# Optimization experiments

Hardware: AMD Instinct MI355X
Metric: run time of the kernel (lower is better)

The kernel has to match this reference:

```python
import jax, jax.numpy as jnp
import numpy as np

NUM_HEAD = 8
HIDDEN = 1024


def setup_inputs() -> dict:
    key = jax.random.key(0)
    ks = jax.random.split(key, 7)
    B, Q, K = 2, 256, 256
    return {
        "query": jax.random.normal(ks[0], (B, Q, HIDDEN), jnp.float32),
        "keys": jax.random.normal(ks[1], (B, K, HIDDEN), jnp.float32),
        "values": jax.random.normal(ks[2], (B, K, HIDDEN), jnp.float32),
        "mask": jax.random.randint(ks[3], (B, K), 0, 2, jnp.int32),
        "W_q": jax.random.normal(ks[4], (HIDDEN, HIDDEN), jnp.float32),
        "W_k": jax.random.normal(ks[5], (HIDDEN, HIDDEN), jnp.float32),
        "V_a": jax.random.normal(ks[6], (HIDDEN,), jnp.float32),
    }


def reference(query, keys, values, mask, W_q, W_k, V_a):
    B, Q, H = query.shape
    K = keys.shape[1]
    h_q = query @ W_q                                   # [B,Q,H]
    h_k = keys @ W_k                                    # [B,K,H]
    # additive (Bahdanau) scores, split hidden into heads and sum per head
    h = jnp.tanh(h_q[:, :, None, :] + h_k[:, None, :, :]) * V_a   # [B,Q,K,H]
    logits = h.reshape(B, Q, K, NUM_HEAD, H // NUM_HEAD).sum(-1)  # [B,Q,K,h]
    logits = jnp.transpose(logits, (0, 3, 1, 2))        # [B,h,Q,K]
    penalty = (1.0 - mask.astype(jnp.float32)) * 99.0   # [B,K]
    logits = logits - penalty[:, None, None, :]
    weights = jax.nn.softmax(logits, axis=-1)           # [B,h,Q,K]
    v = values.reshape(B, K, NUM_HEAD, H // NUM_HEAD)   # [B,K,h,d]
    ctx = jnp.einsum('bhqk,bkhd->bqhd', weights, v).reshape(B, Q, H)
    return ctx, weights
```

## Files before the change

kernel.cpp:

```cpp
#include <hip/hip_runtime.h>
#include <hip/hip_bf16.h>


#define TANH_SCALE 2.88539008177792681472f
#define LOG2E      1.44269504088896340736f

typedef __attribute__((ext_vector_type(8))) short bf16x8_t;
typedef __attribute__((ext_vector_type(4))) float f32x4_t;

__device__ inline ushort bf16_rne(float f) {
  unsigned u = __float_as_uint(f);
  u += 0x7FFFu + ((u >> 16) & 1u);
  return (ushort)(u >> 16);
}
__device__ inline float bf16_to_f(ushort h) { return __uint_as_float((unsigned)h << 16); }
__device__ inline void split1(float v, ushort& hi, ushort& lo) {
  hi = bf16_rne(v);
  lo = bf16_rne(v - bf16_to_f(hi));
}

__global__ __launch_bounds__(256) void prep(
    const float* __restrict__ query, const float* __restrict__ keys,
    const float* __restrict__ Wq, const float* __restrict__ Wk,
    ushort* __restrict__ qhi, ushort* __restrict__ qlo,
    ushort* __restrict__ khi, ushort* __restrict__ klo,
    ushort* __restrict__ wqthi, ushort* __restrict__ wqtlo,
    ushort* __restrict__ wkthi, ushort* __restrict__ wktlo)
{
  __shared__ float t[64][65];
  const int bid = blockIdx.x, tid = threadIdx.x;
  if (bid < 1024) {
    const int z = bid >> 9;
    const float* in = z ? keys : query;
    ushort* hi = z ? khi : qhi;
    ushort* lo = z ? klo : qlo;
    const size_t i = ((size_t)(bid & 511) * 256 + tid) * 4;
    float4 v = *(const float4*)(in + i);
    ushort h0, h1, h2, h3, l0, l1, l2, l3;
    split1(v.x, h0, l0); split1(v.y, h1, l1);
    split1(v.z, h2, l2); split1(v.w, h3, l3);
    *(ushort4*)(hi + i) = make_ushort4(h0, h1, h2, h3);
    *(ushort4*)(lo + i) = make_ushort4(l0, l1, l2, l3);
  } else {
    const int idx = bid - 1024;
    const int z = idx >> 8;
    const float* W = z ? Wk : Wq;
    ushort* thi = z ? wkthi : wqthi;
    ushort* tlo = z ? wktlo : wqtlo;
    const int n0 = (idx & 15) * 64, h0 = ((idx >> 4) & 15) * 64;
    const int r = tid >> 4, c = (tid & 15) * 4;
#pragma unroll
    for (int i = 0; i < 4; ++i) {
      const int rr = r + i * 16;
      float4 wv = *(const float4*)(W + (size_t)(h0 + rr) * 1024 + n0 + c);
      t[rr][c + 0] = wv.x; t[rr][c + 1] = wv.y;
      t[rr][c + 2] = wv.z; t[rr][c + 3] = wv.w;
    }
    __syncthreads();
#pragma unroll
    for (int i = 0; i < 4; ++i) {
      const int rr = r + i * 16;
      ushort h0v, h1v, h2v, h3v, l0v, l1v, l2v, l3v;
      split1(t[c + 0][rr] * TANH_SCALE, h0v, l0v);
      split1(t[c + 1][rr] * TANH_SCALE, h1v, l1v);
      split1(t[c + 2][rr] * TANH_SCALE, h2v, l2v);
      split1(t[c + 3][rr] * TANH_SCALE, h3v, l3v);
      *(ushort4*)(thi + (size_t)(n0 + rr) * 1024 + h0 + c) = make_ushort4(h0v, h1v, h2v, h3v);
      *(ushort4*)(tlo + (size_t)(n0 + rr) * 1024 + h0 + c) = make_ushort4(l0v, l1v, l2v, l3v);
    }
  }
}

__global__ __launch_bounds__(256) void gemm_mfma(
    const ushort* __restrict__ qhi, const ushort* __restrict__ qlo,
    const ushort* __restrict__ khi, const ushort* __restrict__ klo,
    const ushort* __restrict__ wqthi, const ushort* __restrict__ wqtlo,
    const ushort* __restrict__ wkthi, const ushort* __restrict__ wktlo,
    float* __restrict__ hq_f, float* __restrict__ hkT)
{
  const int z = blockIdx.y;
  const int bid = blockIdx.x;
  int m0, n0, ldc;
  const ushort *Ah_g, *Al_g, *Bh_g, *Bl_g;
  float* C;
  if (z == 0) {
    m0 = (bid >> 4) * 64; n0 = (bid & 15) * 64; ldc = 1024;
    Ah_g = qhi; Al_g = qlo; Bh_g = wqthi; Bl_g = wqtlo; C = hq_f;
  } else {
    m0 = (bid >> 3) * 64; n0 = (bid & 7) * 64; ldc = 512;
    Ah_g = wkthi; Al_g = wktlo; Bh_g = khi; Bl_g = klo; C = hkT;
  }

  __shared__ __align__(16) ushort Ah[64 * 40];
  __shared__ __align__(16) ushort Al[64 * 40];
  __shared__ __align__(16) ushort Bh[64 * 40];
  __shared__ __align__(16) ushort Bl[64 * 40];

  const int tid = threadIdx.x;
  const int srow = tid >> 2, skc = (tid & 3) * 8;
  const size_t gA = (size_t)(m0 + srow) * 1024 + skc;
  const size_t gB = (size_t)(n0 + srow) * 1024 + skc;
  const int soff = srow * 40 + skc;

  uint4 rah = *(const uint4*)(Ah_g + gA);
  uint4 ral = *(const uint4*)(Al_g + gA);
  uint4 rbh = *(const uint4*)(Bh_g + gB);
  uint4 rbl = *(const uint4*)(Bl_g + gB);

  const int w = __builtin_amdgcn_readfirstlane(tid >> 6);
  const int lane = tid & 63;
  const int wm = (w >> 1) * 32, wn = (w & 1) * 32;
  const int fr = lane & 15, kg = lane >> 4;
  const int aoff = (wm + fr) * 40 + kg * 8;
  const int boff = (wn + fr) * 40 + kg * 8;

  f32x4_t acc[2][2] = {};

  for (int kk = 0; kk < 1024; kk += 32) {
    __syncthreads();
    *(uint4*)(Ah + soff) = rah;
    *(uint4*)(Al + soff) = ral;
    *(uint4*)(Bh + soff) = rbh;
    *(uint4*)(Bl + soff) = rbl;
    __syncthreads();

    if (kk + 32 < 1024) {
      rah = *(const uint4*)(Ah_g + gA + kk + 32);
      ral = *(const uint4*)(Al_g + gA + kk + 32);
      rbh = *(const uint4*)(Bh_g + gB + kk + 32);
      rbl = *(const uint4*)(Bl_g + gB + kk + 32);
    }

    bf16x8_t ah0 = *(const bf16x8_t*)(Ah + aoff);
    bf16x8_t ah1 = *(const bf16x8_t*)(Ah + aoff + 16 * 40);
    bf16x8_t al0 = *(const bf16x8_t*)(Al + aoff);
    bf16x8_t al1 = *(const bf16x8_t*)(Al + aoff + 16 * 40);
    bf16x8_t bh0 = *(const bf16x8_t*)(Bh + boff);
    bf16x8_t bh1 = *(const bf16x8_t*)(Bh + boff + 16 * 40);
    bf16x8_t bl0 = *(const bf16x8_t*)(Bl + boff);
    bf16x8_t bl1 = *(const bf16x8_t*)(Bl + boff + 16 * 40);

    acc[0][0] = __builtin_amdgcn_mfma_f32_16x16x32_bf16(ah0, bh0, acc[0][0], 0, 0, 0);
    acc[0][1] = __builtin_amdgcn_mfma_f32_16x16x32_bf16(ah0, bh1, acc[0][1], 0, 0, 0);
    acc[1][0] = __builtin_amdgcn_mfma_f32_16x16x32_bf16(ah1, bh0, acc[1][0], 0, 0, 0);
    acc[1][1] = __builtin_amdgcn_mfma_f32_16x16x32_bf16(ah1, bh1, acc[1][1], 0, 0, 0);
    acc[0][0] = __builtin_amdgcn_mfma_f32_16x16x32_bf16(ah0, bl0, acc[0][0], 0, 0, 0);
    acc[0][1] = __builtin_amdgcn_mfma_f32_16x16x32_bf16(ah0, bl1, acc[0][1], 0, 0, 0);
    acc[1][0] = __builtin_amdgcn_mfma_f32_16x16x32_bf16(ah1, bl0, acc[1][0], 0, 0, 0);
    acc[1][1] = __builtin_amdgcn_mfma_f32_16x16x32_bf16(ah1, bl1, acc[1][1], 0, 0, 0);
    acc[0][0] = __builtin_amdgcn_mfma_f32_16x16x32_bf16(al0, bh0, acc[0][0], 0, 0, 0);
    acc[0][1] = __builtin_amdgcn_mfma_f32_16x16x32_bf16(al0, bh1, acc[0][1], 0, 0, 0);
    acc[1][0] = __builtin_amdgcn_mfma_f32_16x16x32_bf16(al1, bh0, acc[1][0], 0, 0, 0);
    acc[1][1] = __builtin_amdgcn_mfma_f32_16x16x32_bf16(al1, bh1, acc[1][1], 0, 0, 0);
  }

#pragma unroll
  for (int fm = 0; fm < 2; ++fm)
#pragma unroll
    for (int fn = 0; fn < 2; ++fn) {
      const int col = n0 + wn + fn * 16 + fr;
#pragma unroll
      for (int j = 0; j < 4; ++j) {
        const int row = m0 + wm + fm * 16 + kg * 4 + j;
        C[(size_t)row * ldc + col] = acc[fm][fn][j];
      }
    }
}

#define COMP(vk, hq0v, hq1v, vad)                                     \
  {                                                                   \
    float e0 = __builtin_amdgcn_exp2f(hq0v + vk.x);                   \
    float e1 = __builtin_amdgcn_exp2f(hq0v + vk.y);                   \
    float e2 = __builtin_amdgcn_exp2f(hq0v + vk.z);                   \
    float e3 = __builtin_amdgcn_exp2f(hq0v + vk.w);                   \
    acc00 += vad * __builtin_amdgcn_rcpf(e0 + 1.0f);                  \
    acc01 += vad * __builtin_amdgcn_rcpf(e1 + 1.0f);                  \
    acc02 += vad * __builtin_amdgcn_rcpf(e2 + 1.0f);                  \
    acc03 += vad * __builtin_amdgcn_rcpf(e3 + 1.0f);                  \
    float f0 = __builtin_amdgcn_exp2f(hq1v + vk.x);                   \
    float f1 = __builtin_amdgcn_exp2f(hq1v + vk.y);                   \
    float f2 = __builtin_amdgcn_exp2f(hq1v + vk.z);                   \
    float f3 = __builtin_amdgcn_exp2f(hq1v + vk.w);                   \
    acc10 += vad * __builtin_amdgcn_rcpf(f0 + 1.0f);                  \
    acc11 += vad * __builtin_amdgcn_rcpf(f1 + 1.0f);                  \
    acc12 += vad * __builtin_amdgcn_rcpf(f2 + 1.0f);                  \
    acc13 += vad * __builtin_amdgcn_rcpf(f3 + 1.0f);                  \
  }

__global__ __launch_bounds__(256) void attn_fused(
    const float* __restrict__ hq_f, const float* __restrict__ hkT,
    const float* __restrict__ Va, const int* __restrict__ mask,
    const float* __restrict__ values,
    float* __restrict__ weights, float* __restrict__ ctx)
{
  __shared__ __align__(16) float w_lds[8 * 256];
  const int tid = threadIdx.x;
  const int lane = tid & 63;
  const int w = __builtin_amdgcn_readfirstlane(tid >> 6);
  const int bid = blockIdx.x;
  const int hb = bid >> 5;
  const int b = hb & 1, h = hb >> 1;
  const int qt = (bid & 31) * 8;
  const int q0 = qt + w * 2;

  int4 mk = *(const int4*)(mask + b * 256 + 4 * lane);
  const float pen0 = 99.0f * (1.0f - (float)mk.x);
  const float pen1 = 99.0f * (1.0f - (float)mk.y);
  const float pen2 = 99.0f * (1.0f - (float)mk.z);
  const float pen3 = 99.0f * (1.0f - (float)mk.w);

  float ssum = Va[h * 128 + lane] + Va[h * 128 + 64 + lane];
#pragma unroll
  for (int off = 32; off; off >>= 1) ssum += __shfl_xor(ssum, off, 64);

  const float* hkbase = hkT + (size_t)(h * 128) * 512 + b * 256 + 4 * lane;
  const float* hqr0 = hq_f + (size_t)(b * 256 + q0) * 1024 + h * 128;
  const float* hqr1 = hqr0 + 1024;
  const float* vap = Va + h * 128;

  float acc00 = 0.f, acc01 = 0.f, acc02 = 0.f, acc03 = 0.f;
  float acc10 = 0.f, acc11 = 0.f, acc12 = 0.f, acc13 = 0.f;

  float4 vk0 = *(const float4*)(hkbase + 0 * 512);
  float4 vk1 = *(const float4*)(hkbase + 1 * 512);
  float4 vk2 = *(const float4*)(hkbase + 2 * 512);
  float4 vk3 = *(const float4*)(hkbase + 3 * 512);
  float4 hqA = *(const float4*)(hqr0);
  float4 hqB = *(const float4*)(hqr1);
  float4 va4 = *(const float4*)(vap);

  for (int g = 0; g < 32; ++g) {
    float4 nvk0, nvk1, nvk2, nvk3, nhqA, nhqB, nva4;
    if (g < 31) {
      const float* hb2 = hkbase + (size_t)(4 * g + 4) * 512;
      nvk0 = *(const float4*)(hb2 + 0 * 512);
      nvk1 = *(const float4*)(hb2 + 1 * 512);
      nvk2 = *(const float4*)(hb2 + 2 * 512);
      nvk3 = *(const float4*)(hb2 + 3 * 512);
      nhqA = *(const float4*)(hqr0 + 4 * g + 4);
      nhqB = *(const float4*)(hqr1 + 4 * g + 4);
      nva4 = *(const float4*)(vap + 4 * g + 4);
    }
    COMP(vk0, hqA.x, hqB.x, va4.x);
    COMP(vk1, hqA.y, hqB.y, va4.y);
    COMP(vk2, hqA.z, hqB.z, va4.z);
    COMP(vk3, hqA.w, hqB.w, va4.w);
    if (g < 31) {
      vk0 = nvk0; vk1 = nvk1; vk2 = nvk2; vk3 = nvk3;
      hqA = nhqA; hqB = nhqB; va4 = nva4;
    }
  }

  float4 L0, L1;
  L0.x = ssum - 2.0f * acc00 - pen0;
  L0.y = ssum - 2.0f * acc01 - pen1;
  L0.z = ssum - 2.0f * acc02 - pen2;
  L0.w = ssum - 2.0f * acc03 - pen3;
  L1.x = ssum - 2.0f * acc10 - pen0;
  L1.y = ssum - 2.0f * acc11 - pen1;
  L1.z = ssum - 2.0f * acc12 - pen2;
  L1.w = ssum - 2.0f * acc13 - pen3;

  float m0 = fmaxf(fmaxf(L0.x, L0.y), fmaxf(L0.z, L0.w));
  float m1 = fmaxf(fmaxf(L1.x, L1.y), fmaxf(L1.z, L1.w));
#pragma unroll
  for (int off = 32; off; off >>= 1) {
    m0 = fmaxf(m0, __shfl_xor(m0, off, 64));
    m1 = fmaxf(m1, __shfl_xor(m1, off, 64));
  }
  float4 P0, P1;
  P0.x = __builtin_amdgcn_exp2f((L0.x - m0) * LOG2E);
  P0.y = __builtin_amdgcn_exp2f((L0.y - m0) * LOG2E);
  P0.z = __builtin_amdgcn_exp2f((L0.z - m0) * LOG2E);
  P0.w = __builtin_amdgcn_exp2f((L0.w - m0) * LOG2E);
  P1.x = __builtin_amdgcn_exp2f((L1.x - m1) * LOG2E);
  P1.y = __builtin_amdgcn_exp2f((L1.y - m1) * LOG2E);
  P1.z = __builtin_amdgcn_exp2f((L1.z - m1) * LOG2E);
  P1.w = __builtin_amdgcn_exp2f((L1.w - m1) * LOG2E);
  float s0 = (P0.x + P0.y) + (P0.z + P0.w);
  float s1 = (P1.x + P1.y) + (P1.z + P1.w);
#pragma unroll
  for (int off = 32; off; off >>= 1) {
    s0 += __shfl_xor(s0, off, 64);
    s1 += __shfl_xor(s1, off, 64);
  }
  float inv0 = 1.0f / s0, inv1 = 1.0f / s1;
  P0.x *= inv0; P0.y *= inv0; P0.z *= inv0; P0.w *= inv0;
  P1.x *= inv1; P1.y *= inv1; P1.z *= inv1; P1.w *= inv1;

  float* wp = weights + ((size_t)((b * 8 + h) * 256) + q0) * 256 + 4 * lane;
  *(float4*)(wp) = P0;
  *(float4*)(wp + 256) = P1;
  *(float4*)&w_lds[(w * 2 + 0) * 256 + 4 * lane] = P0;
  *(float4*)&w_lds[(w * 2 + 1) * 256 + 4 * lane] = P1;
  __syncthreads();

  const int q = tid >> 5, dq = tid & 31;
  const float* vb = values + (size_t)(b * 256) * 1024 + h * 128 + dq * 4;
  const float* wrow = w_lds + q * 256;
  float4 accE = make_float4(0, 0, 0, 0), accO = make_float4(0, 0, 0, 0);
#pragma unroll 4
  for (int k = 0; k < 256; k += 2) {
    float4 v0 = *(const float4*)&vb[k * 1024];
    float4 v1 = *(const float4*)&vb[(k + 1) * 1024];
    float w0 = wrow[k], w1 = wrow[k + 1];
    accE.x += w0 * v0.x; accE.y += w0 * v0.y; accE.z += w0 * v0.z; accE.w += w0 * v0.w;
    accO.x += w1 * v1.x; accO.y += w1 * v1.y; accO.z += w1 * v1.z; accO.w += w1 * v1.w;
  }
  float4 o;
  o.x = accE.x + accO.x; o.y = accE.y + accO.y; o.z = accE.z + accO.z; o.w = accE.w + accO.w;
  *(float4*)&ctx[(size_t)(b * 256 + qt + q) * 1024 + h * 128 + dq * 4] = o;
}

extern "C" void kernel_launch(void* const* d_in, const int* in_sizes, int n_in,
                              void* d_out, int out_size, void* d_ws, size_t ws_size,
                              hipStream_t stream) {
  const float* query  = (const float*)d_in[0];
  const float* keys   = (const float*)d_in[1];
  const float* values = (const float*)d_in[2];
  const int*   mask   = (const int*)d_in[3];
  const float* Wq     = (const float*)d_in[4];
  const float* Wk     = (const float*)d_in[5];
  const float* Va     = (const float*)d_in[6];

  float* ctx     = (float*)d_out;
  float* weights = ctx + 524288;

  ushort* qhi   = (ushort*)d_ws;
  ushort* qlo   = qhi + 524288;
  ushort* khi   = qlo + 524288;
  ushort* klo   = khi + 524288;
  ushort* wqthi = klo + 524288;
  ushort* wqtlo = wqthi + 1048576;
  ushort* wkthi = wqtlo + 1048576;
  ushort* wktlo = wkthi + 1048576;
  float*  hq_f  = (float*)(wktlo + 1048576);
  float*  hkT   = hq_f + 524288;

  prep<<<dim3(1536), 256, 0, stream>>>(query, keys, Wq, Wk,
                                       qhi, qlo, khi, klo,
                                       wqthi, wqtlo, wkthi, wktlo);
  gemm_mfma<<<dim3(128, 2), 256, 0, stream>>>(qhi, qlo, khi, klo,
                                              wqthi, wqtlo, wkthi, wktlo, hq_f, hkT);
  attn_fused<<<dim3(512), 256, 0, stream>>>(hq_f, hkT, Va, mask, values, weights, ctx);
}
```

Measured before the change: 73.10 us.

## Split attention work across more blocks with key-halved waves and cross-wave reductions

Each block now handles 2 queries instead of 8, and the two waves per query each cover half of the keys (2 keys per lane instead of 4 keys across 2 queries). Softmax max and sum are combined across wave pairs through shared memory, and the PV product is split over key quarters with a shuffle plus LDS reduction. This raises the grid from 512 to 2048 blocks to improve occupancy and latency hiding in the tanh-heavy score loop. In exchange, the hq and hk loads are reused less, synchronisation goes up, and the weight stores are narrower.

```diff
diff --git a/kernel.cpp b/kernel.cpp
--- a/kernel.cpp
+++ b/kernel.cpp
@@ -167,149 +167,139 @@
     }
 }
 
-#define COMP(vk, hq0v, hq1v, vad)                                     \
-  {                                                                   \
-    float e0 = __builtin_amdgcn_exp2f(hq0v + vk.x);                   \
-    float e1 = __builtin_amdgcn_exp2f(hq0v + vk.y);                   \
-    float e2 = __builtin_amdgcn_exp2f(hq0v + vk.z);                   \
-    float e3 = __builtin_amdgcn_exp2f(hq0v + vk.w);                   \
-    acc00 += vad * __builtin_amdgcn_rcpf(e0 + 1.0f);                  \
-    acc01 += vad * __builtin_amdgcn_rcpf(e1 + 1.0f);                  \
-    acc02 += vad * __builtin_amdgcn_rcpf(e2 + 1.0f);                  \
-    acc03 += vad * __builtin_amdgcn_rcpf(e3 + 1.0f);                  \
-    float f0 = __builtin_amdgcn_exp2f(hq1v + vk.x);                   \
-    float f1 = __builtin_amdgcn_exp2f(hq1v + vk.y);                   \
-    float f2 = __builtin_amdgcn_exp2f(hq1v + vk.z);                   \
-    float f3 = __builtin_amdgcn_exp2f(hq1v + vk.w);                   \
-    acc10 += vad * __builtin_amdgcn_rcpf(f0 + 1.0f);                  \
-    acc11 += vad * __builtin_amdgcn_rcpf(f1 + 1.0f);                  \
-    acc12 += vad * __builtin_amdgcn_rcpf(f2 + 1.0f);                  \
-    acc13 += vad * __builtin_amdgcn_rcpf(f3 + 1.0f);                  \
-  }
-
 __global__ __launch_bounds__(256) void attn_fused(
     const float* __restrict__ hq_f, const float* __restrict__ hkT,
     const float* __restrict__ Va, const int* __restrict__ mask,
     const float* __restrict__ values,
     float* __restrict__ weights, float* __restrict__ ctx)
 {
-  __shared__ __align__(16) float w_lds[8 * 256];
+  __shared__ float red_m[4];
+  __shared__ float red_s[4];
+  __shared__ __align__(16) float w_lds[2][256];
+  __shared__ __align__(16) float pv_part[4][32][4];
+
   const int tid = threadIdx.x;
   const int lane = tid & 63;
   const int w = __builtin_amdgcn_readfirstlane(tid >> 6);
+  const int r = w >> 1, kh = w & 1;
   const int bid = blockIdx.x;
-  const int hb = bid >> 5;
-  const int b = hb & 1, h = hb >> 1;
-  const int qt = (bid & 31) * 8;
-  const int q0 = qt + w * 2;
-
-  int4 mk = *(const int4*)(mask + b * 256 + 4 * lane);
+  const int bh = bid >> 7;
+  const int b = bh & 1, h = bh >> 1;
+  const int q = (bid & 127) * 2 + r;
+  const int k0 = kh * 128 + 2 * lane;
+
+  const int2 mk = *(const int2*)(mask + b * 256 + k0);
   const float pen0 = 99.0f * (1.0f - (float)mk.x);
   const float pen1 = 99.0f * (1.0f - (float)mk.y);
-  const float pen2 = 99.0f * (1.0f - (float)mk.z);
-  const float pen3 = 99.0f * (1.0f - (float)mk.w);
 
   float ssum = Va[h * 128 + lane] + Va[h * 128 + 64 + lane];
 #pragma unroll
   for (int off = 32; off; off >>= 1) ssum += __shfl_xor(ssum, off, 64);
 
-  const float* hkbase = hkT + (size_t)(h * 128) * 512 + b * 256 + 4 * lane;
-  const float* hqr0 = hq_f + (size_t)(b * 256 + q0) * 1024 + h * 128;
-  const float* hqr1 = hqr0 + 1024;
+  const float* ekb = hkT + (size_t)(h * 128) * 512 + b * 256 + k0;
+  const float* hqp = hq_f + (size_t)(b * 256 + q) * 1024 + h * 128;
   const float* vap = Va + h * 128;
 
-  float acc00 = 0.f, acc01 = 0.f, acc02 = 0.f, acc03 = 0.f;
-  float acc10 = 0.f, acc11 = 0.f, acc12 = 0.f, acc13 = 0.f;
-
-  float4 vk0 = *(const float4*)(hkbase + 0 * 512);
-  float4 vk1 = *(const float4*)(hkbase + 1 * 512);
-  float4 vk2 = *(const float4*)(hkbase + 2 * 512);
-  float4 vk3 = *(const float4*)(hkbase + 3 * 512);
-  float4 hqA = *(const float4*)(hqr0);
-  float4 hqB = *(const float4*)(hqr1);
+  float a0e = 0.f, a0o = 0.f, a1e = 0.f, a1o = 0.f;
+
+  float2 e0 = *(const float2*)(ekb + 0 * 512);
+  float2 e1 = *(const float2*)(ekb + 1 * 512);
+  float2 e2 = *(const float2*)(ekb + 2 * 512);
+  float2 e3 = *(const float2*)(ekb + 3 * 512);
+  float4 hq4 = *(const float4*)(hqp);
   float4 va4 = *(const float4*)(vap);
 
   for (int g = 0; g < 32; ++g) {
-    float4 nvk0, nvk1, nvk2, nvk3, nhqA, nhqB, nva4;
+    float2 n0v, n1v, n2v, n3v; float4 nhq, nva;
     if (g < 31) {
-      const float* hb2 = hkbase + (size_t)(4 * g + 4) * 512;
-      nvk0 = *(const float4*)(hb2 + 0 * 512);
-      nvk1 = *(const float4*)(hb2 + 1 * 512);
-      nvk2 = *(const float4*)(hb2 + 2 * 512);
-      nvk3 = *(const float4*)(hb2 + 3 * 512);
-      nhqA = *(const float4*)(hqr0 + 4 * g + 4);
-      nhqB = *(const float4*)(hqr1 + 4 * g + 4);
-      nva4 = *(const float4*)(vap + 4 * g + 4);
-    }
-    COMP(vk0, hqA.x, hqB.x, va4.x);
-    COMP(vk1, hqA.y, hqB.y, va4.y);
-    COMP(vk2, hqA.z, hqB.z, va4.z);
-    COMP(vk3, hqA.w, hqB.w, va4.w);
+      const float* nb = ekb + (size_t)(4 * g + 4) * 512;
+      n0v = *(const float2*)(nb + 0 * 512);
+      n1v = *(const float2*)(nb + 1 * 512);
+      n2v = *(const float2*)(nb + 2 * 512);
+      n3v = *(const float2*)(nb + 3 * 512);
+      nhq = *(const float4*)(hqp + 4 * g + 4);
+      nva = *(const float4*)(vap + 4 * g + 4);
+    }
+    {
+      float t0 = __builtin_amdgcn_exp2f(hq4.x + e0.x);
+      float t1 = __builtin_amdgcn_exp2f(hq4.x + e0.y);
+      a0e += va4.x * __builtin_amdgcn_rcpf(t0 + 1.0f);
+      a1e += va4.x * __builtin_amdgcn_rcpf(t1 + 1.0f);
+      float u0 = __builtin_amdgcn_exp2f(hq4.y + e1.x);
+      float u1 = __builtin_amdgcn_exp2f(hq4.y + e1.y);
+      a0o += va4.y * __builtin_amdgcn_rcpf(u0 + 1.0f);
+      a1o += va4.y * __builtin_amdgcn_rcpf(u1 + 1.0f);
+      float v0 = __builtin_amdgcn_exp2f(hq4.z + e2.x);
+      float v1 = __builtin_amdgcn_exp2f(hq4.z + e2.y);
+      a0e += va4.z * __builtin_amdgcn_rcpf(v0 + 1.0f);
+      a1e += va4.z * __builtin_amdgcn_rcpf(v1 + 1.0f);
+      float x0 = __builtin_amdgcn_exp2f(hq4.w + e3.x);
+      float x1 = __builtin_amdgcn_exp2f(hq4.w + e3.y);
+      a0o += va4.w * __builtin_amdgcn_rcpf(x0 + 1.0f);
+      a1o += va4.w * __builtin_amdgcn_rcpf(x1 + 1.0f);
+    }
     if (g < 31) {
-      vk0 = nvk0; vk1 = nvk1; vk2 = nvk2; vk3 = nvk3;
-      hqA = nhqA; hqB = nhqB; va4 = nva4;
-    }
-  }
-
-  float4 L0, L1;
-  L0.x = ssum - 2.0f * acc00 - pen0;
-  L0.y = ssum - 2.0f * acc01 - pen1;
-  L0.z = ssum - 2.0f * acc02 - pen2;
-  L0.w = ssum - 2.0f * acc03 - pen3;
-  L1.x = ssum - 2.0f * acc10 - pen0;
-  L1.y = ssum - 2.0f * acc11 - pen1;
-  L1.z = ssum - 2.0f * acc12 - pen2;
-  L1.w = ssum - 2.0f * acc13 - pen3;
-
-  float m0 = fmaxf(fmaxf(L0.x, L0.y), fmaxf(L0.z, L0.w));
-  float m1 = fmaxf(fmaxf(L1.x, L1.y), fmaxf(L1.z, L1.w));
-#pragma unroll
-  for (int off = 32; off; off >>= 1) {
-    m0 = fmaxf(m0, __shfl_xor(m0, off, 64));
-    m1 = fmaxf(m1, __shfl_xor(m1, off, 64));
-  }
-  float4 P0, P1;
-  P0.x = __builtin_amdgcn_exp2f((L0.x - m0) * LOG2E);
-  P0.y = __builtin_amdgcn_exp2f((L0.y - m0) * LOG2E);
-  P0.z = __builtin_amdgcn_exp2f((L0.z - m0) * LOG2E);
-  P0.w = __builtin_amdgcn_exp2f((L0.w - m0) * LOG2E);
-  P1.x = __builtin_amdgcn_exp2f((L1.x - m1) * LOG2E);
-  P1.y = __builtin_amdgcn_exp2f((L1.y - m1) * LOG2E);
-  P1.z = __builtin_amdgcn_exp2f((L1.z - m1) * LOG2E);
-  P1.w = __builtin_amdgcn_exp2f((L1.w - m1) * LOG2E);
-  float s0 = (P0.x + P0.y) + (P0.z + P0.w);
-  float s1 = (P1.x + P1.y) + (P1.z + P1.w);
-#pragma unroll
-  for (int off = 32; off; off >>= 1) {
-    s0 += __shfl_xor(s0, off, 64);
-    s1 += __shfl_xor(s1, off, 64);
-  }
-  float inv0 = 1.0f / s0, inv1 = 1.0f / s1;
-  P0.x *= inv0; P0.y *= inv0; P0.z *= inv0; P0.w *= inv0;
-  P1.x *= inv1; P1.y *= inv1; P1.z *= inv1; P1.w *= inv1;
-
-  float* wp = weights + ((size_t)((b * 8 + h) * 256) + q0) * 256 + 4 * lane;
-  *(float4*)(wp) = P0;
-  *(float4*)(wp + 256) = P1;
-  *(float4*)&w_lds[(w * 2 + 0) * 256 + 4 * lane] = P0;
-  *(float4*)&w_lds[(w * 2 + 1) * 256 + 4 * lane] = P1;
+      e0 = n0v; e1 = n1v; e2 = n2v; e3 = n3v;
+      hq4 = nhq; va4 = nva;
+    }
+  }
+
+  const float l0 = ssum - 2.0f * (a0e + a0o) - pen0;
+  const float l1 = ssum - 2.0f * (a1e + a1o) - pen1;
+
+  float mx = fmaxf(l0, l1);
+#pragma unroll
+  for (int off = 32; off; off >>= 1) mx = fmaxf(mx, __shfl_xor(mx, off, 64));
+  if (lane == 0) red_m[w] = mx;
   __syncthreads();
-
-  const int q = tid >> 5, dq = tid & 31;
-  const float* vb = values + (size_t)(b * 256) * 1024 + h * 128 + dq * 4;
-  const float* wrow = w_lds + q * 256;
+  const float m = fmaxf(mx, red_m[w ^ 1]);
+
+  float p0 = __builtin_amdgcn_exp2f((l0 - m) * LOG2E);
+  float p1 = __builtin_amdgcn_exp2f((l1 - m) * LOG2E);
+  float s = p0 + p1;
+#pragma unroll
+  for (int off = 32; off; off >>= 1) s += __shfl_xor(s, off, 64);
+  if (lane == 0) red_s[w] = s;
+  __syncthreads();
+  const float invS = 1.0f / (s + red_s[w ^ 1]);
+  p0 *= invS; p1 *= invS;
+
+  float* wp = weights + ((size_t)((b * 8 + h) * 256) + q) * 256 + k0;
+  wp[0] = p0; wp[1] = p1;
+  w_lds[r][k0] = p0; w_lds[r][k0 + 1] = p1;
+  __syncthreads();
+
+  const int d4 = lane & 31, ks = lane >> 5;
+  const float* vb = values + (size_t)(b * 256 + kh * 128 + ks * 64) * 1024 + h * 128 + d4 * 4;
+  const float* wr = &w_lds[r][kh * 128 + ks * 64];
   float4 accE = make_float4(0, 0, 0, 0), accO = make_float4(0, 0, 0, 0);
 #pragma unroll 4
-  for (int k = 0; k < 256; k += 2) {
+  for (int k = 0; k < 64; k += 2) {
     float4 v0 = *(const float4*)&vb[k * 1024];
     float4 v1 = *(const float4*)&vb[(k + 1) * 1024];
-    float w0 = wrow[k], w1 = wrow[k + 1];
+    float w0 = wr[k], w1 = wr[k + 1];
     accE.x += w0 * v0.x; accE.y += w0 * v0.y; accE.z += w0 * v0.z; accE.w += w0 * v0.w;
     accO.x += w1 * v1.x; accO.y += w1 * v1.y; accO.z += w1 * v1.z; accO.w += w1 * v1.w;
   }
-  float4 o;
-  o.x = accE.x + accO.x; o.y = accE.y + accO.y; o.z = accE.z + accO.z; o.w = accE.w + accO.w;
-  *(float4*)&ctx[(size_t)(b * 256 + qt + q) * 1024 + h * 128 + dq * 4] = o;
+  float4 a;
+  a.x = accE.x + accO.x; a.y = accE.y + accO.y;
+  a.z = accE.z + accO.z; a.w = accE.w + accO.w;
+  a.x += __shfl_xor(a.x, 32, 64);
+  a.y += __shfl_xor(a.y, 32, 64);
+  a.z += __shfl_xor(a.z, 32, 64);
+  a.w += __shfl_xor(a.w, 32, 64);
+  if (lane < 32) *(float4*)&pv_part[w][d4][0] = a;
+  __syncthreads();
+
+  if (tid < 64) {
+    const int rr = tid >> 5, dd = tid & 31;
+    float4 pa = *(const float4*)&pv_part[2 * rr][dd][0];
+    float4 pb = *(const float4*)&pv_part[2 * rr + 1][dd][0];
+    float4 o;
+    o.x = pa.x + pb.x; o.y = pa.y + pb.y; o.z = pa.z + pb.z; o.w = pa.w + pb.w;
+    const int qg = (bid & 127) * 2 + rr;
+    *(float4*)&ctx[(size_t)(b * 256 + qg) * 1024 + h * 128 + dd * 4] = o;
+  }
 }
 
 extern "C" void kernel_launch(void* const* d_in, const int* in_sizes, int n_in,
@@ -342,5 +332,5 @@
                                        wqthi, wqtlo, wkthi, wktlo);
   gemm_mfma<<<dim3(128, 2), 256, 0, stream>>>(qhi, qlo, khi, klo,
                                               wqthi, wqtlo, wkthi, wktlo, hq_f, hkT);
-  attn_fused<<<dim3(512), 256, 0, stream>>>(hq_f, hkT, Va, mask, values, weights, ctx);
-}
+  attn_fused<<<dim3(2048), 256, 0, stream>>>(hq_f, hkT, Va, mask, values, weights, ctx);
+}
```

Measured after the change: 76.60 us. +4.8%, slower.
